# Performance work log

Measured on AMD Instinct MI355X. Metric: run time of the kernel, lower is better.

## Reference

```python
import jax, jax.numpy as jnp
import numpy as np

HID, OUT, HEADS, DIM_HEAD, TOPK, CHUNK = 512, 5, 8, 64, 8, 32
INNER = HEADS * DIM_HEAD  # 512
EPS = 1e-5


def setup_inputs():
    key = jax.random.key(0)
    ks = jax.random.split(key, 12)
    def p(k, shape, fan_in):
        return (jax.random.normal(k, shape, jnp.float32) / np.sqrt(fan_in).astype(np.float32))
    return {
        'x': jax.random.normal(ks[0], (32, 3, 32, 32), jnp.float32),
        'queries': jax.random.normal(ks[1], (4, 128, HID), jnp.float32),
        'memories': jax.random.normal(ks[2], (4, 20000, HID), jnp.float32),
        'mask': jnp.ones((4, 20000), bool),
        'conv1_w': p(ks[3], (16, 3, 3, 3), 27), 'conv1_b': jnp.zeros((16,), jnp.float32),
        'conv2_w': p(ks[4], (32, 16, 3, 3), 144), 'conv2_b': jnp.zeros((32,), jnp.float32),
        'fc1_w': p(ks[5], (32 * 8 * 8, HID), 2048), 'fc1_b': jnp.zeros((HID,), jnp.float32),
        'sq_w': p(ks[6], (HID, HID), HID), 'sq_b': jnp.zeros((HID,), jnp.float32),
        'sk_w': p(ks[7], (HID, HID), HID), 'sk_b': jnp.zeros((HID,), jnp.float32),
        'q_w': p(ks[8], (HID, INNER), HID),
        'kv_w': p(ks[9], (HID, 2 * INNER), HID),
        'out_w': p(ks[10], (INNER, HID), INNER), 'out_b': jnp.zeros((HID,), jnp.float32),
        'fc2_w': p(ks[11], (HID, OUT), HID), 'fc2_b': jnp.zeros((OUT,), jnp.float32),
    }


def _maxpool2(h):
    return jax.lax.reduce_window(h, -jnp.inf, jax.lax.max, (1, 1, 2, 2), (1, 1, 2, 2), 'VALID')


def _forward(x, queries, memories, mask, conv1_w, conv1_b, conv2_w, conv2_b,
             fc1_w, fc1_b, sq_w, sq_b, sk_w, sk_b, q_w, kv_w, out_w, out_b, fc2_w, fc2_b):
    # --- CNN branch: faithfully computed, but its output is discarded by the
    # original forward (x is overwritten by the attention output) ---
    dn = ('NCHW', 'OIHW', 'NCHW')
    h = jax.lax.conv_general_dilated(x, conv1_w, (1, 1), 'SAME', dimension_numbers=dn)
    h = _maxpool2(jax.nn.relu(h + conv1_b[None, :, None, None]))
    h = jax.lax.conv_general_dilated(h, conv2_w, (1, 1), 'SAME', dimension_numbers=dn)
    h = _maxpool2(jax.nn.relu(h + conv2_b[None, :, None, None]))
    h = h.reshape(h.shape[0], -1) @ fc1_w + fc1_b  # (B, 512), dead value (matches torch code)
    _ = h

    # --- HTMAttention ---
    b, qn, dim = queries.shape
    scale = dim ** -0.5  # chunk-scoring scale uses full dim
    mem = memories.reshape(b, -1, CHUNK, dim)            # (b, n, c, d)
    mk = mask.reshape(b, -1, CHUNK)                      # (b, n, c)

    # masked mean-pool summaries per chunk
    denom = mk.sum(-1, keepdims=True).astype(mem.dtype)  # (b, n, 1)
    summarized = jnp.where(mk[..., None], mem, 0.0).sum(2) / (denom + EPS)  # (b, n, d)

    sq = queries @ sq_w + sq_b                           # (b, i, d)
    sk = jax.lax.stop_gradient(summarized) @ sk_w + sk_b # (b, n, d)
    logits = jnp.einsum('bid,bnd->bin', sq, sk) * scale  # (b, i, n)
    neg = -jnp.finfo(logits.dtype).max
    logits = jnp.where(mk.any(-1)[:, None, :], logits, neg)

    topk_logits, topk_idx = jax.lax.top_k(logits, TOPK)  # (b, i, k)
    weights = jax.nn.softmax(topk_logits, axis=-1)       # (b, i, k)

    bidx = jnp.arange(b)[:, None, None]
    selected = mem[bidx, topk_idx]                       # (b, i, k, c, d) gather of chunks
    sel_mask = mk[bidx, topk_idx]                        # (b, i, k, c)

    # sinusoidal position over chunk positions (reversed arange, step-2 freqs)
    inv_freqs = 1e4 ** (-jnp.arange(0, dim, 2.0) / dim)              # (d/2,)
    sinu = jnp.arange(CHUNK - 1, -1, -1.0)[:, None] * inv_freqs      # (c, d/2)
    pos = jnp.concatenate([jnp.sin(sinu), jnp.cos(sinu)], -1)        # (c, d)
    selected = selected + pos

    # within-chunk multi-head attention (memories detached, as in original)
    mems_in = jax.lax.stop_gradient(selected)
    q = (queries @ q_w).reshape(b, qn, HEADS, DIM_HEAD) * (DIM_HEAD ** -0.5)  # (b,i,h,e)
    kv = (mems_in @ kv_w).reshape(b, qn, TOPK, CHUNK, 2, HEADS, DIM_HEAD)
    kk, vv = kv[..., 0, :, :], kv[..., 1, :, :]          # (b,i,k,c,h,e)

    sim = jnp.einsum('bihe,bikche->bhikc', q, kk)        # (b,h,i,k,c)
    sim = jnp.where(sel_mask[:, None], sim, neg)
    attn = jax.nn.softmax(sim, axis=-1)
    o = jnp.einsum('bhikc,bikche->bikhe', attn, vv).reshape(b, qn, TOPK, INNER)
    o = o @ out_w + out_b                                # (b, i, k, d)

    htm = (o * weights[..., None]).sum(2)                # (b, i, d)
    return htm @ fc2_w + fc2_b                           # (b, i, OUT)


def reference(x, queries, memories, mask, conv1_w, conv1_b, conv2_w, conv2_b,
              fc1_w, fc1_b, sq_w, sq_b, sk_w, sk_b, q_w, kv_w, out_w, out_b, fc2_w, fc2_b):
    return _forward(x, queries, memories, mask, conv1_w, conv1_b, conv2_w, conv2_b,
                    fc1_w, fc1_b, sq_w, sq_b, sk_w, sk_b, q_w, kv_w, out_w, out_b, fc2_w, fc2_b)
```

## Files before the change

kernel.cpp:

```cpp
#include <hip/hip_runtime.h>
#include <hip/hip_bf16.h>
#include <float.h>
#include <math.h>

#define NB      4
#define QN      128
#define HID     512
#define NMEM    20000
#define MPAD    20096
#define NCHUNK  625
#define CHUNK   32
#define HEADS   8
#define DHEAD   64
#define TOPKK   8
#define NKV     1024
#define GLD     64
#define LOGIT_SCALE 0.044194173824159216f
#define W2LD    576
#define STROWS  520
#define LGLD    640
#define TLD     4096

typedef __attribute__((ext_vector_type(8))) short bf16x8;
typedef __attribute__((ext_vector_type(4))) short bf16x4;
typedef __attribute__((ext_vector_type(4))) float f32x4;

__device__ __forceinline__ short f2bf(float f){
  __hip_bfloat16 h = __float2bfloat16(f);
  return *reinterpret_cast<short*>(&h);
}
__device__ __forceinline__ float bf2f(unsigned short s){
  __hip_bfloat16 h;
  *reinterpret_cast<unsigned short*>(&h) = s;
  return __bfloat162float(h);
}
__device__ __forceinline__ bool mask_at(const void* m, int flag, long i){
  return flag ? (((const unsigned char*)m)[i] != 0)
              : (((const int*)m)[i] != 0);
}
__device__ __forceinline__ void gload16(const void* g, void* l){
  __builtin_amdgcn_global_load_lds((const __attribute__((address_space(1))) void*)g,
                                   (__attribute__((address_space(3))) void*)l, 16, 0, 0);
}

__global__ __launch_bounds__(256) void bigsetup_kernel(const float* __restrict__ skw,
                                                       const void* __restrict__ mask,
                                                       const float* __restrict__ out_w,
                                                       const float* __restrict__ out_b,
                                                       const float* __restrict__ fc2_w,
                                                       const float* __restrict__ fc2_b,
                                                       const float* __restrict__ sq_w,
                                                       const float* __restrict__ sq_b,
                                                       const float* __restrict__ sk_b,
                                                       const float* __restrict__ q_w,
                                                       const float* __restrict__ kvw,
                                                       const float* __restrict__ queries,
                                                       float* __restrict__ skwT,
                                                       float* __restrict__ pos,
                                                       int* __restrict__ flagp,
                                                       float* __restrict__ bfold,
                                                       float* __restrict__ W2buf,
                                                       float* __restrict__ v2,
                                                       float* __restrict__ gbuf,
                                                       unsigned short* __restrict__ wqk,
                                                       unsigned short* __restrict__ qb,
                                                       unsigned short* __restrict__ PB){
  __shared__ float sm[12480];
  int sub = blockIdx.x;
  int t = threadIdx.x;
  if (sub < 64){
    float (*tile)[65] = (float(*)[65])sm;
    int c = t & 63, rbase = t >> 6;
    int e0 = (sub >> 3) * 64, j0 = (sub & 7) * 64;
#pragma unroll
    for (int j = 0; j < 16; ++j){
      int r = rbase + j * 4;
      tile[r][c] = skw[(long)(e0 + r) * 512 + j0 + c];
    }
    __syncthreads();
#pragma unroll
    for (int j = 0; j < 16; ++j){
      int rj = rbase + j * 4;
      skwT[(long)(j0 + rj) * 512 + e0 + c] = tile[c][rj];
    }
  } else if (sub < 128){
    int s = sub - 64;
    int cc = s >> 1;
    int d = (s & 1) * 256 + t;
    int j = (d < 256) ? d : d - 256;
    float invf = expf(-((2.0f * (float)j) / 512.0f) * 9.2103403719761836f);
    float arg = (float)(31 - cc) * invf;
    pos[cc * 512 + d] = (d < 256) ? sinf(arg) : cosf(arg);
    if (s == 0 && t == 0){
      const unsigned char* mb = (const unsigned char*)mask;
      *flagp = (mb[1] != 0) ? 1 : 0;
    }
  } else if (sub == 128){
    if (t < 5){
      float sb = 0.f;
      for (int k = 0; k < 512; ++k) sb += out_b[k] * fc2_w[k * 5 + t];
      bfold[t] = sb + fc2_b[t];
    }
  } else if (sub < 134){
    int s = sub - 129;
    if (s < 2){
      int d = s * 256 + t;
      float acc = 0.f;
      for (int j = 0; j < 512; ++j) acc += sq_w[(long)d * 512 + j] * sk_b[j];
      W2buf[(long)d * W2LD + 512] = acc;
      for (int cc = 513; cc < W2LD; ++cc) W2buf[(long)d * W2LD + cc] = 0.f;
    } else if (s < 4){
      int e = (s - 2) * 256 + t;
      float acc = 0.f;
      for (int j = 0; j < 512; ++j) acc += skw[(long)e * 512 + j] * sq_b[j];
      v2[e] = acc;
    } else {
      __shared__ float g[256];
      g[t] = sq_b[t] * sk_b[t] + sq_b[t + 256] * sk_b[t + 256];
      __syncthreads();
      for (int d = 128; d >= 1; d >>= 1){
        if (t < d) g[t] += g[t + d];
        __syncthreads();
      }
      if (t == 0) gbuf[0] = g[0];
    }
  } else if (sub < 390){
    int bx = sub - 134;
    int h = bx >> 5, rem2 = bx & 31, dp = rem2 >> 2, dd = rem2 & 3;
    int dpr0 = dp * 64, dd0 = dd * 128;
    float (*Akv)[65] = (float(*)[65])sm;
    float (*Bq)[65]  = (float(*)[65])(sm + 64 * 65);
    for (int idx = t; idx < 64 * 64; idx += 256){
      int r = idx >> 6, e = idx & 63;
      Akv[r][e] = kvw[(long)(dpr0 + r) * NKV + h * 64 + e];
    }
    for (int idx = t; idx < 128 * 64; idx += 256){
      int r = idx >> 6, e = idx & 63;
      Bq[r][e] = q_w[(long)(dd0 + r) * 512 + h * 64 + e];
    }
    __syncthreads();
    int ty = t >> 4, tx = t & 15;
    float acc[4][8] = {};
    for (int e = 0; e < 64; ++e){
      float a0 = Akv[ty * 4 + 0][e], a1 = Akv[ty * 4 + 1][e];
      float a2 = Akv[ty * 4 + 2][e], a3 = Akv[ty * 4 + 3][e];
      float b[8];
#pragma unroll
      for (int v = 0; v < 8; ++v) b[v] = Bq[tx * 8 + v][e];
#pragma unroll
      for (int v = 0; v < 8; ++v){
        acc[0][v] += a0 * b[v];
        acc[1][v] += a1 * b[v];
        acc[2][v] += a2 * b[v];
        acc[3][v] += a3 * b[v];
      }
    }
#pragma unroll
    for (int u = 0; u < 4; ++u)
#pragma unroll
      for (int v = 0; v < 8; ++v)
        wqk[(long)(h * 512 + dpr0 + ty * 4 + u) * 512 + dd0 + tx * 8 + v] =
            (unsigned short)f2bf(acc[u][v] * 0.125f);
  } else if (sub < 646){
    long idx = (long)(sub - 390) * 256 + t;
    float4 v = *(const float4*)(queries + idx * 4);
    ushort4 o;
    o.x = (unsigned short)f2bf(v.x);
    o.y = (unsigned short)f2bf(v.y);
    o.z = (unsigned short)f2bf(v.z);
    o.w = (unsigned short)f2bf(v.w);
    *(ushort4*)(qb + idx * 4) = o;
  } else {
    int row = sub - 646;
    if (row < 40){
      int h = row / 5, j = row - h * 5;
      __shared__ float wfc[64];
      if (t < 64){
        const float* owr = out_w + (long)(h * 64 + t) * 512;
        float s = 0.f;
        for (int k = 0; k < 512; ++k) s += owr[k] * fc2_w[k * 5 + j];
        wfc[t] = s;
      }
      __syncthreads();
      for (int d = t; d < 512; d += 256){
        const float* kr = kvw + (long)d * NKV + 512 + h * 64;
        float s = 0.f;
#pragma unroll
        for (int e = 0; e < 64; ++e) s += kr[e] * wfc[e];
        PB[(long)row * 512 + d] = (unsigned short)f2bf(s);
      }
    } else {
      for (int d = t; d < 512; d += 256) PB[(long)row * 512 + d] = 0;
    }
  }
}

__global__ __launch_bounds__(512) void prepsum_kernel(const float* __restrict__ memories,
                                                      const float* __restrict__ pos,
                                                      const void* __restrict__ mask,
                                                      const int* __restrict__ flagp,
                                                      unsigned short* __restrict__ abf_all,
                                                      float* __restrict__ summ,
                                                      float* __restrict__ chunkden){
  int n = blockIdx.x, b = blockIdx.y;
  int t = threadIdx.x;
  unsigned short* abf = abf_all + (long)b * MPAD * 512;
  if (n == NCHUNK){
    for (int idx = t; idx < 96 * 128; idx += 512){
      ushort4 z = {0, 0, 0, 0};
      *(ushort4*)(abf + (long)(NMEM + (idx >> 7)) * 512 + (long)(idx & 127) * 4) = z;
    }
    return;
  }
  long mbase = (long)b * NMEM + (long)n * CHUNK;
  int flag = *flagp;
  bool mybit = mask_at(mask, flag, mbase + (t & 31));
  unsigned int m32 = (unsigned int)__ballot(mybit);
  float den = (float)__popc(m32);
  int rh = t >> 6;
  int c8 = t & 63;
  const float* base = memories + mbase * HID + c8 * 8;
  const float* pbase = pos + c8 * 8;
  float4 va[4], vb[4], pa[4], pb[4];
#pragma unroll
  for (int j = 0; j < 4; ++j){
    va[j] = *(const float4*)(base + (long)(rh + 8 * j) * HID);
    vb[j] = *(const float4*)(base + (long)(rh + 8 * j) * HID + 4);
  }
#pragma unroll
  for (int j = 0; j < 4; ++j){
    pa[j] = *(const float4*)(pbase + (rh + 8 * j) * HID);
    pb[j] = *(const float4*)(pbase + (rh + 8 * j) * HID + 4);
  }
#pragma unroll
  for (int j = 0; j < 4; ++j){
    union { unsigned short u[8]; int4 v; } o;
    o.u[0] = (unsigned short)f2bf(va[j].x + pa[j].x);
    o.u[1] = (unsigned short)f2bf(va[j].y + pa[j].y);
    o.u[2] = (unsigned short)f2bf(va[j].z + pa[j].z);
    o.u[3] = (unsigned short)f2bf(va[j].w + pa[j].w);
    o.u[4] = (unsigned short)f2bf(vb[j].x + pb[j].x);
    o.u[5] = (unsigned short)f2bf(vb[j].y + pb[j].y);
    o.u[6] = (unsigned short)f2bf(vb[j].z + pb[j].z);
    o.u[7] = (unsigned short)f2bf(vb[j].w + pb[j].w);
    *(int4*)(abf + (long)(n * CHUNK + rh + 8 * j) * 512 + c8 * 8) = o.v;
  }
  float acc[8] = {};
#pragma unroll
  for (int j = 0; j < 4; ++j){
    if (m32 & (1u << (rh + 8 * j))){
      acc[0] += va[j].x; acc[1] += va[j].y; acc[2] += va[j].z; acc[3] += va[j].w;
      acc[4] += vb[j].x; acc[5] += vb[j].y; acc[6] += vb[j].z; acc[7] += vb[j].w;
    }
  }
  __shared__ float red[512][9];
#pragma unroll
  for (int k = 0; k < 8; ++k) red[t][k] = acc[k];
  __syncthreads();
  if (rh == 0){
    float s[8] = {};
    for (int g = 0; g < 8; ++g)
#pragma unroll
      for (int k = 0; k < 8; ++k) s[k] += red[g * 64 + c8][k];
    float dv = den + 1e-5f;
    float4 s0 = {s[0] / dv, s[1] / dv, s[2] / dv, s[3] / dv};
    float4 s1 = {s[4] / dv, s[5] / dv, s[6] / dv, s[7] / dv};
    float* srow = summ + ((long)b * NCHUNK + n) * 512 + c8 * 8;
    *(float4*)srow = s0;
    *(float4*)(srow + 4) = s1;
    if (t == 0) chunkden[b * NCHUNK + n] = den;
  }
}

__global__ __launch_bounds__(256) void gt_gemm(const unsigned short* __restrict__ abf_all,
                                               const unsigned short* __restrict__ PB,
                                               unsigned short* __restrict__ g_all,
                                               const unsigned short* __restrict__ Aq,
                                               const unsigned short* __restrict__ Bw,
                                               float* __restrict__ T,
                                               const float* __restrict__ sq_w,
                                               const float* __restrict__ skwT,
                                               float* __restrict__ W2buf){
  __shared__ unsigned short pool[20480];
  int blk = blockIdx.x;
  int tid = threadIdx.x, wid = tid >> 6, lane = tid & 63;
  int lr = lane & 15, lg = lane >> 4;
  int scol = (lane & 3) << 3;
  int srow = wid * 16 + (lane >> 2);

  if (blk < 316){
    int bb = blk / 79, g = blk - bb * 79;
    const unsigned short* A = abf_all + (size_t)bb * MPAD * 512;
    unsigned short* gout = g_all + (size_t)bb * MPAD * GLD;
    unsigned short* As[2] = { pool, pool + 8192 };
    unsigned short* Bs[2] = { pool + 16384, pool + 18432 };
    long rbase = (long)g * 256 + srow;
    long ra0 = rbase;       if (ra0 > MPAD - 1) ra0 = MPAD - 1;
    long ra1 = rbase + 64;  if (ra1 > MPAD - 1) ra1 = MPAD - 1;
    long ra2 = rbase + 128; if (ra2 > MPAD - 1) ra2 = MPAD - 1;
    long ra3 = rbase + 192; if (ra3 > MPAD - 1) ra3 = MPAD - 1;
    const unsigned short* gA0 = A + ra0 * 512 + scol;
    const unsigned short* gA1 = A + ra1 * 512 + scol;
    const unsigned short* gA2 = A + ra2 * 512 + scol;
    const unsigned short* gA3 = A + ra3 * 512 + scol;
    const unsigned short* gB0 = PB + (long)srow * 512 + scol;
    int lA0 = (wid * 16) * 32, lA1 = (64 + wid * 16) * 32;
    int lA2 = (128 + wid * 16) * 32, lA3 = (192 + wid * 16) * 32;
    int lB0 = (wid * 16) * 32;

    f32x4 acc[4][4];
#pragma unroll
    for (int i = 0; i < 4; ++i)
#pragma unroll
      for (int j = 0; j < 4; ++j) acc[i][j] = (f32x4)0.f;

#define GSTAGE(B, K0) { gload16(gA0 + (K0), &As[B][lA0]); gload16(gA1 + (K0), &As[B][lA1]); \
                        gload16(gA2 + (K0), &As[B][lA2]); gload16(gA3 + (K0), &As[B][lA3]); \
                        gload16(gB0 + (K0), &Bs[B][lB0]); }
#define GCOMPUTE(B) { bf16x8 af[4], bfv[4]; \
  _Pragma("unroll") for (int mi = 0; mi < 4; ++mi) af[mi]  = *(const bf16x8*)&As[B][(wid * 64 + mi * 16 + lr) * 32 + lg * 8]; \
  _Pragma("unroll") for (int ni = 0; ni < 4; ++ni) bfv[ni] = *(const bf16x8*)&Bs[B][(ni * 16 + lr) * 32 + lg * 8]; \
  _Pragma("unroll") for (int mi = 0; mi < 4; ++mi) \
    _Pragma("unroll") for (int ni = 0; ni < 4; ++ni) \
      acc[mi][ni] = __builtin_amdgcn_mfma_f32_16x16x32_bf16(af[mi], bfv[ni], acc[mi][ni], 0, 0, 0); }

    GSTAGE(0, 0);
    __syncthreads();
#pragma unroll 1
    for (int tt = 0; tt < 16; tt += 2){
      if (tt + 1 < 16) GSTAGE(1, (tt + 1) * 32);
      GCOMPUTE(0);
      __syncthreads();
      if (tt + 2 < 16) GSTAGE(0, (tt + 2) * 32);
      GCOMPUTE(1);
      __syncthreads();
    }
#undef GSTAGE
#undef GCOMPUTE

#pragma unroll
    for (int mi = 0; mi < 4; ++mi)
#pragma unroll
      for (int ni = 0; ni < 4; ++ni)
#pragma unroll
        for (int rr = 0; rr < 4; ++rr){
          long gr = (long)g * 256 + wid * 64 + mi * 16 + lg * 4 + rr;
          int gn = ni * 16 + lr;
          if (gr < MPAD)
            gout[gr * GLD + gn] = (unsigned short)f2bf(acc[mi][ni][rr]);
        }
  } else if (blk < 444){
    int L2 = blk - 316;
    int panel = L2 >> 5, nb = L2 & 31;
    int m0 = panel << 7, n0 = nb << 7;
    int wr = wid >> 1, wc = wid & 1;
    unsigned short* As[2] = { pool, pool + 4096 };
    unsigned short* Bs[2] = { pool + 8192, pool + 12288 };
    const unsigned short* gA0 = Aq + (long)(m0 + srow) * 512 + scol;
    const unsigned short* gA1 = gA0 + 64 * 512;
    const unsigned short* gB0 = Bw + (long)(n0 + srow) * 512 + scol;
    const unsigned short* gB1 = gB0 + 64 * 512;
    int lofs0 = (wid * 16) * 32;
    int lofs1 = (64 + wid * 16) * 32;

    f32x4 acc[4][4];
#pragma unroll
    for (int i = 0; i < 4; ++i)
#pragma unroll
      for (int j = 0; j < 4; ++j) acc[i][j] = (f32x4)0.f;

#define TSTAGE(B, K0) { gload16(gA0 + (K0), &As[B][lofs0]); gload16(gA1 + (K0), &As[B][lofs1]); \
                        gload16(gB0 + (K0), &Bs[B][lofs0]); gload16(gB1 + (K0), &Bs[B][lofs1]); }
#define TCOMPUTE(B) { bf16x8 af[4], bfv[4]; \
  _Pragma("unroll") for (int mi = 0; mi < 4; ++mi) af[mi]  = *(const bf16x8*)&As[B][(wr * 64 + mi * 16 + lr) * 32 + lg * 8]; \
  _Pragma("unroll") for (int ni = 0; ni < 4; ++ni) bfv[ni] = *(const bf16x8*)&Bs[B][(wc * 64 + ni * 16 + lr) * 32 + lg * 8]; \
  _Pragma("unroll") for (int mi = 0; mi < 4; ++mi) \
    _Pragma("unroll") for (int ni = 0; ni < 4; ++ni) \
      acc[mi][ni] = __builtin_amdgcn_mfma_f32_16x16x32_bf16(af[mi], bfv[ni], acc[mi][ni], 0, 0, 0); }

    TSTAGE(0, 0);
    __syncthreads();
#pragma unroll 1
    for (int tt = 0; tt < 16; tt += 2){
      if (tt + 1 < 16) TSTAGE(1, (tt + 1) * 32);
      TCOMPUTE(0);
      __syncthreads();
      if (tt + 2 < 16) TSTAGE(0, (tt + 2) * 32);
      TCOMPUTE(1);
      __syncthreads();
    }
#undef TSTAGE
#undef TCOMPUTE

#pragma unroll
    for (int mi = 0; mi < 4; ++mi)
#pragma unroll
      for (int ni = 0; ni < 4; ++ni)
#pragma unroll
        for (int rr = 0; rr < 4; ++rr){
          int gr = m0 + wr * 64 + mi * 16 + lg * 4 + rr;
          int gn = n0 + wc * 64 + ni * 16 + lr;
          T[(long)gr * TLD + gn] = acc[mi][ni][rr];
        }
  } else {
    int bx3 = blk - 444;
    int rt = bx3 & 63, nt2 = bx3 >> 6;
    int r0 = rt * 8 + wid * 2;
    int nn = nt2 * 64 + lane;
    const float* a0 = sq_w + (long)r0 * 512;
    const float* bp = skwT + nn;
    float acc0 = 0.f, acc1 = 0.f;
#pragma unroll 4
    for (int k = 0; k < 512; k += 4){
      float b0 = bp[(long)k * 512];
      float b1 = bp[(long)(k + 1) * 512];
      float b2 = bp[(long)(k + 2) * 512];
      float b3 = bp[(long)(k + 3) * 512];
      float4 a;
      a = *(const float4*)(a0 + k);
      acc0 += a.x * b0 + a.y * b1 + a.z * b2 + a.w * b3;
      a = *(const float4*)(a0 + 512 + k);
      acc1 += a.x * b0 + a.y * b1 + a.z * b2 + a.w * b3;
    }
    W2buf[(long)r0 * W2LD + nn]       = acc0;
    W2buf[(long)(r0 + 1) * W2LD + nn] = acc1;
  }
}

__global__ __launch_bounds__(256) void ustb_kernel(const float* __restrict__ queries,
                                                   const float* __restrict__ W2buf,
                                                   float* __restrict__ u_ext,
                                                   const float* __restrict__ summ,
                                                   const float* __restrict__ v2,
                                                   const float* __restrict__ gbuf,
                                                   float* __restrict__ summText,
                                                   float* __restrict__ betag){
  int blk = blockIdx.x;
  int t = threadIdx.x;
  if (blk < 576){
    int ax = blk & 63, ay = blk >> 6;
    int lane = t & 63, w = t >> 6;
    int r0 = ax * 8 + w * 2;
    int n  = ay * 64 + lane;
    const float* a0 = queries + (long)r0 * 512;
    const float* bp = W2buf + n;
    float acc0 = 0.f, acc1 = 0.f;
#pragma unroll 4
    for (int k = 0; k < 512; k += 4){
      float b0 = bp[(long)k * W2LD];
      float b1 = bp[(long)(k + 1) * W2LD];
      float b2 = bp[(long)(k + 2) * W2LD];
      float b3 = bp[(long)(k + 3) * W2LD];
      float4 a;
      a = *(const float4*)(a0 + k);
      acc0 += a.x * b0 + a.y * b1 + a.z * b2 + a.w * b3;
      a = *(const float4*)(a0 + 512 + k);
      acc1 += a.x * b0 + a.y * b1 + a.z * b2 + a.w * b3;
    }
    u_ext[(long)r0 * W2LD + n]       = acc0;
    u_ext[(long)(r0 + 1) * W2LD + n] = acc1;
  } else if (blk < 896){
    __shared__ float tile[64][65];
    int b2 = blk - 576;
    int b = b2 / 80; int rem = b2 % 80;
    int n0 = (rem / 8) * 64, e0 = (rem % 8) * 64;
    int c = t & 63, rbase = t >> 6;
#pragma unroll
    for (int j = 0; j < 16; ++j){
      int r = rbase + j * 4;
      int n = n0 + r;
      tile[r][c] = (n < NCHUNK) ? summ[((long)b * NCHUNK + n) * 512 + e0 + c] : 0.f;
    }
    __syncthreads();
#pragma unroll
    for (int j = 0; j < 16; ++j){
      int re = rbase + j * 4;
      summText[(long)b * STROWS * LGLD + (long)(e0 + re) * LGLD + n0 + c] = tile[c][re];
    }
  } else if (blk < 900){
    int b = blk - 896;
    for (int idx = t; idx < 8 * LGLD; idx += 256){
      int e = idx / LGLD, n = idx - e * LGLD;
      summText[(long)b * STROWS * LGLD + (long)(512 + e) * LGLD + n] = (e == 0) ? 1.f : 0.f;
    }
  } else {
    int bb = blk - 900;
    int w = t >> 6, lane = t & 63;
    int row = bb * 4 + w;
    const float* r = summ + (long)row * 512;
    float s = 0.f;
#pragma unroll
    for (int c = 0; c < 8; ++c) s += r[lane + 64 * c] * v2[lane + 64 * c];
    for (int d = 32; d >= 1; d >>= 1) s += __shfl_xor(s, d, 64);
    if (lane == 0){
      int b = row / NCHUNK, n = row % NCHUNK;
      betag[b * LGLD + n] = s + gbuf[0];
    }
  }
}

__global__ __launch_bounds__(256) void logits_nn(const float* __restrict__ u_ext,
                                                 const float* __restrict__ summText,
                                                 const float* __restrict__ betag,
                                                 const float* __restrict__ chunkden,
                                                 float* __restrict__ logits){
  int b = blockIdx.z;
  int tid = threadIdx.x;
  int lane = tid & 63, w = tid >> 6;
  int r0 = blockIdx.x * 8 + w * 2;
  int n  = blockIdx.y * 64 + lane;
  const float* a0 = u_ext + ((long)b * QN + r0) * W2LD;
  const float* bp = summText + (long)b * STROWS * LGLD + n;
  float acc0 = 0.f, acc1 = 0.f;
#pragma unroll 4
  for (int k = 0; k < STROWS; k += 4){
    float b0 = bp[(long)k * LGLD];
    float b1 = bp[(long)(k + 1) * LGLD];
    float b2 = bp[(long)(k + 2) * LGLD];
    float b3 = bp[(long)(k + 3) * LGLD];
    float4 a;
    a = *(const float4*)(a0 + k);
    acc0 += a.x * b0 + a.y * b1 + a.z * b2 + a.w * b3;
    a = *(const float4*)(a0 + W2LD + k);
    acc1 += a.x * b0 + a.y * b1 + a.z * b2 + a.w * b3;
  }
  if (n < NCHUNK){
    float bet = betag[b * LGLD + n];
    bool dead = (chunkden[b * NCHUNK + n] <= 0.f);
    float v0 = (acc0 + bet) * LOGIT_SCALE;
    float v1 = (acc1 + bet) * LOGIT_SCALE;
    if (dead){ v0 = v1 = -FLT_MAX; }
    long base = ((long)b * QN + r0) * LGLD + n;
    logits[base]        = v0;
    logits[base + LGLD] = v1;
  }
}

__global__ __launch_bounds__(256) void topk_kernel(const float* __restrict__ logits,
                                                   int* __restrict__ topi_out,
                                                   float* __restrict__ wts_out){
  int row = blockIdx.x;
  __shared__ float lds[NCHUNK];
  __shared__ float wv[4];
  __shared__ int   wi[4];
  __shared__ float topv[TOPKK];
  __shared__ int   topi[TOPKK];
  int t = threadIdx.x;
  int lane = t & 63, w = t >> 6;
  for (int idx = t; idx < NCHUNK; idx += 256) lds[idx] = logits[(long)row * LGLD + idx];
  __syncthreads();
  for (int it = 0; it < TOPKK; ++it){
    float bv = -INFINITY; int bi = 0x7fffffff;
    for (int idx = t; idx < NCHUNK; idx += 256){
      float v = lds[idx];
      if (v > bv){ bv = v; bi = idx; }
    }
    for (int d = 32; d >= 1; d >>= 1){
      float ov = __shfl_xor(bv, d, 64);
      int   oi = __shfl_xor(bi, d, 64);
      if (ov > bv || (ov == bv && oi < bi)){ bv = ov; bi = oi; }
    }
    if (lane == 0){ wv[w] = bv; wi[w] = bi; }
    __syncthreads();
    if (t == 0){
      float fb = wv[0]; int fi = wi[0];
      for (int j = 1; j < 4; ++j){
        if (wv[j] > fb || (wv[j] == fb && wi[j] < fi)){ fb = wv[j]; fi = wi[j]; }
      }
      topv[it] = fb; topi[it] = fi; lds[fi] = -INFINITY;
    }
    __syncthreads();
  }
  if (t == 0){
    float m = topv[0];
    for (int r = 1; r < TOPKK; ++r) m = fmaxf(m, topv[r]);
    float e[TOPKK], s = 0.f;
    for (int r = 0; r < TOPKK; ++r){ e[r] = expf(topv[r] - m); s += e[r]; }
    for (int r = 0; r < TOPKK; ++r){
      wts_out[(long)row * TOPKK + r] = e[r] / s;
      topi_out[(long)row * TOPKK + r] = topi[r];
    }
  }
}

#define ALDP 516
__global__ __launch_bounds__(256) void attn5_kernel(const float* __restrict__ T,
                                                    const unsigned short* __restrict__ abf_all,
                                                    const unsigned short* __restrict__ g_all,
                                                    const int* __restrict__ topidx,
                                                    const float* __restrict__ wts,
                                                    const void* __restrict__ mask,
                                                    const int* __restrict__ flagp,
                                                    float* __restrict__ osc5){
  int bx = blockIdx.x;
  int bb = bx >> 10, rem = bx & 1023;
  int i = rem >> 3, k = rem & 7;
  const unsigned short* abf = abf_all + (size_t)bb * MPAD * 512;
  const unsigned short* gb  = g_all + (size_t)bb * MPAD * GLD;
  int t = threadIdx.x;
  __shared__ unsigned short A_lds[32 * ALDP];
  __shared__ float T_lds[TLD];
  __shared__ float red[4][5];
  int flag = *flagp;
  long sel = ((long)(bb * QN + i)) * TOPKK + k;
  int chunk = topidx[sel];
  float w8 = wts[sel];
  const float* Trow = T + (long)(bb * QN + i) * TLD;
  for (int idx = t; idx < 1024; idx += 256)
    *(float4*)&T_lds[idx * 4] = *(const float4*)&Trow[idx * 4];
  {
    int r = t >> 3, cb = (t & 7) * 64;
    const unsigned short* src = abf + (long)(chunk * CHUNK + r) * 512 + cb;
    unsigned short* dst = &A_lds[r * ALDP + cb];
#pragma unroll
    for (int j = 0; j < 8; ++j){
      bf16x8 a8 = *(const bf16x8*)(src + j * 8);
      bf16x4 lo = {a8[0], a8[1], a8[2], a8[3]};
      bf16x4 hi = {a8[4], a8[5], a8[6], a8[7]};
      *(bf16x4*)(dst + j * 8)     = lo;
      *(bf16x4*)(dst + j * 8 + 4) = hi;
    }
  }
  __syncthreads();
  int h = t >> 5, c = t & 31;
  const unsigned short* arow = &A_lds[c * ALDP];
  const float* tp = &T_lds[h * 512];
  float s = 0.f;
#pragma unroll 4
  for (int e8 = 0; e8 < 64; ++e8){
    bf16x4 alo = *(const bf16x4*)(arow + e8 * 8);
    bf16x4 ahi = *(const bf16x4*)(arow + e8 * 8 + 4);
    float4 ta = *(const float4*)(tp + e8 * 8);
    float4 tb = *(const float4*)(tp + e8 * 8 + 4);
    s += bf2f((unsigned short)alo[0]) * ta.x + bf2f((unsigned short)alo[1]) * ta.y
       + bf2f((unsigned short)alo[2]) * ta.z + bf2f((unsigned short)alo[3]) * ta.w
       + bf2f((unsigned short)ahi[0]) * tb.x + bf2f((unsigned short)ahi[1]) * tb.y
       + bf2f((unsigned short)ahi[2]) * tb.z + bf2f((unsigned short)ahi[3]) * tb.w;
  }
  bool mv = mask_at(mask, flag, (long)bb * NMEM + (long)chunk * CHUNK + c);
  if (!mv) s = -FLT_MAX;
  float m = s;
  for (int d = 16; d >= 1; d >>= 1) m = fmaxf(m, __shfl_xor(m, d, 32));
  float p = expf(s - m);
  float su = p;
  for (int d = 16; d >= 1; d >>= 1) su += __shfl_xor(su, d, 32);
  float att = p / su;
  const unsigned short* grow = gb + (long)(chunk * CHUNK + c) * GLD + h * 5;
  float p0 = att * bf2f(grow[0]);
  float p1 = att * bf2f(grow[1]);
  float p2 = att * bf2f(grow[2]);
  float p3 = att * bf2f(grow[3]);
  float p4 = att * bf2f(grow[4]);
#pragma unroll
  for (int d = 32; d >= 1; d >>= 1){
    p0 += __shfl_xor(p0, d, 64);
    p1 += __shfl_xor(p1, d, 64);
    p2 += __shfl_xor(p2, d, 64);
    p3 += __shfl_xor(p3, d, 64);
    p4 += __shfl_xor(p4, d, 64);
  }
  int w = t >> 6, lane = t & 63;
  if (lane == 0){
    red[w][0] = p0; red[w][1] = p1; red[w][2] = p2; red[w][3] = p3; red[w][4] = p4;
  }
  __syncthreads();
  if (t < 5){
    float tot = red[0][t] + red[1][t] + red[2][t] + red[3][t];
    osc5[sel * 8 + t] = w8 * tot;
  }
}

__global__ __launch_bounds__(64) void final5_kernel(const float* __restrict__ osc5,
                                                    const float* __restrict__ bfold,
                                                    float* __restrict__ out){
  int bi = blockIdx.x;
  int t = threadIdx.x;
  if (t < 5){
    float a = bfold[t];
#pragma unroll
    for (int k = 0; k < TOPKK; ++k) a += osc5[((long)bi * TOPKK + k) * 8 + t];
    out[bi * 5 + t] = a;
  }
}

extern "C" void kernel_launch(void* const* d_in, const int* in_sizes, int n_in,
                              void* d_out, int out_size, void* d_ws, size_t ws_size,
                              hipStream_t stream) {
  const float* queries  = (const float*)d_in[1];
  const float* memories = (const float*)d_in[2];
  const void*  mask     = d_in[3];
  const float* sq_w = (const float*)d_in[10];
  const float* sq_b = (const float*)d_in[11];
  const float* sk_w = (const float*)d_in[12];
  const float* sk_b = (const float*)d_in[13];
  const float* q_w  = (const float*)d_in[14];
  const float* kv_w = (const float*)d_in[15];
  const float* out_w = (const float*)d_in[16];
  const float* out_b = (const float*)d_in[17];
  const float* fc2_w = (const float*)d_in[18];
  const float* fc2_b = (const float*)d_in[19];
  float* out = (float*)d_out;

  char* ws = (char*)d_ws;
  size_t off = 0;
  auto alloc = [&](size_t bytes){ size_t o = off; off += (bytes + 511) & ~(size_t)511; return o; };
  size_t o_sum  = alloc(5120000);
  size_t o_den  = alloc(10240);
  size_t o_pos  = alloc(65536);
  size_t o_bf   = alloc(512);
  size_t o_ti   = alloc(16384);
  size_t o_wt   = alloc(16384);
  size_t o_flag = alloc(512);
  size_t o_w2   = alloc(1179648);
  size_t o_uex  = alloc(1179648);
  size_t o_st   = alloc(5324800);
  size_t o_bg   = alloc(10240);
  size_t o_v2   = alloc(2048);
  size_t o_gm   = alloc(512);
  size_t o_lg   = alloc(1310720);
  size_t o_osc5 = alloc(131072);
  size_t o_skt  = alloc(1048576);
  size_t o_qbf  = alloc(524288);
  size_t o_wqk  = alloc(4194304);
  size_t o_T    = alloc((size_t)NB * QN * TLD * 4);
  size_t o_pb   = alloc(65536);
  size_t o_abf  = alloc((size_t)NB * MPAD * 512 * 2);
  size_t o_g    = alloc((size_t)NB * MPAD * GLD * 2);

  float* summ  = (float*)(ws + o_sum);
  float* den   = (float*)(ws + o_den);
  float* pos   = (float*)(ws + o_pos);
  float* bfold = (float*)(ws + o_bf);
  int*   ti    = (int*)  (ws + o_ti);
  float* wt    = (float*)(ws + o_wt);
  int*   flagp = (int*)  (ws + o_flag);
  float* W2buf = (float*)(ws + o_w2);
  float* u_ext = (float*)(ws + o_uex);
  float* summText = (float*)(ws + o_st);
  float* betag = (float*)(ws + o_bg);
  float* v2    = (float*)(ws + o_v2);
  float* gbuf  = (float*)(ws + o_gm);
  float* logit = (float*)(ws + o_lg);
  float* osc5  = (float*)(ws + o_osc5);
  float* skwT  = (float*)(ws + o_skt);
  unsigned short* qb   = (unsigned short*)(ws + o_qbf);
  unsigned short* wqk  = (unsigned short*)(ws + o_wqk);
  float* Tbuf  = (float*)(ws + o_T);
  unsigned short* PB   = (unsigned short*)(ws + o_pb);
  unsigned short* abf  = (unsigned short*)(ws + o_abf);
  unsigned short* gall = (unsigned short*)(ws + o_g);

  bigsetup_kernel<<<dim3(710), dim3(256), 0, stream>>>(
      sk_w, mask, out_w, out_b, fc2_w, fc2_b, sq_w, sq_b, sk_b, q_w, kv_w, queries,
      skwT, pos, flagp, bfold, W2buf, v2, gbuf, wqk, qb, PB);

  prepsum_kernel<<<dim3(NCHUNK + 1, NB), dim3(512), 0, stream>>>(
      memories, pos, mask, flagp, abf, summ, den);

  gt_gemm<<<dim3(956), dim3(256), 0, stream>>>(
      abf, PB, gall, qb, wqk, Tbuf, sq_w, skwT, W2buf);

  ustb_kernel<<<dim3(1525), dim3(256), 0, stream>>>(
      queries, W2buf, u_ext, summ, v2, gbuf, summText, betag);
  logits_nn<<<dim3(16, 10, NB), dim3(256), 0, stream>>>(u_ext, summText, betag, den, logit);
  topk_kernel<<<dim3(NB * QN), dim3(256), 0, stream>>>(logit, ti, wt);

  attn5_kernel<<<dim3(NB * QN * TOPKK), dim3(256), 0, stream>>>(
      Tbuf, abf, gall, ti, wt, mask, flagp, osc5);
  final5_kernel<<<dim3(NB * QN), dim3(64), 0, stream>>>(osc5, bfold, out);
}
```

Measured before the change: 275.5 us.

## Fold summary transpose into GEMM launch and fuse attention with final reduction

The summary-transpose, constant-row fill and beta dot-product blocks move out of the old ustb kernel and into the gt_gemm launch, because they do not depend on W2buf. The remaining u_ext GEMM becomes its own small kernel. The per-(query, topk) attention kernel and the final reduction kernel are merged: one block per query loops over the 8 selected chunks, loads the T row into LDS once, and writes the output directly. This removes a launch, the osc5 round trip and the repeated T loads. The cost is 8x fewer attention blocks, each doing serial work, which lowers parallelism.

```diff
diff --git a/kernel.cpp b/kernel.cpp
--- a/kernel.cpp
+++ b/kernel.cpp
@@ -280,7 +280,12 @@
                                                float* __restrict__ T,
                                                const float* __restrict__ sq_w,
                                                const float* __restrict__ skwT,
-                                               float* __restrict__ W2buf){
+                                               float* __restrict__ W2buf,
+                                               const float* __restrict__ summ,
+                                               const float* __restrict__ v2,
+                                               const float* __restrict__ gbuf,
+                                               float* __restrict__ summText,
+                                               float* __restrict__ betag){
   __shared__ unsigned short pool[20480];
   int blk = blockIdx.x;
   int tid = threadIdx.x, wid = tid >> 6, lane = tid & 63;
@@ -402,7 +407,7 @@
           int gn = n0 + wc * 64 + ni * 16 + lr;
           T[(long)gr * TLD + gn] = acc[mi][ni][rr];
         }
-  } else {
+  } else if (blk < 956){
     int bx3 = blk - 444;
     int rt = bx3 & 63, nt2 = bx3 >> 6;
     int r0 = rt * 8 + wid * 2;
@@ -424,79 +429,74 @@
     }
     W2buf[(long)r0 * W2LD + nn]       = acc0;
     W2buf[(long)(r0 + 1) * W2LD + nn] = acc1;
-  }
-}
-
-__global__ __launch_bounds__(256) void ustb_kernel(const float* __restrict__ queries,
+  } else {
+    int sb = blk - 956;
+    int t = tid;
+    if (sb < 320){
+      float (*tile)[65] = (float(*)[65])pool;
+      int b = sb / 80; int rem = sb % 80;
+      int n0 = (rem / 8) * 64, e0 = (rem % 8) * 64;
+      int c = t & 63, rbase = t >> 6;
+#pragma unroll
+      for (int j = 0; j < 16; ++j){
+        int r = rbase + j * 4;
+        int n = n0 + r;
+        tile[r][c] = (n < NCHUNK) ? summ[((long)b * NCHUNK + n) * 512 + e0 + c] : 0.f;
+      }
+      __syncthreads();
+#pragma unroll
+      for (int j = 0; j < 16; ++j){
+        int re = rbase + j * 4;
+        summText[(long)b * STROWS * LGLD + (long)(e0 + re) * LGLD + n0 + c] = tile[c][re];
+      }
+    } else if (sb < 324){
+      int b = sb - 320;
+      for (int idx = t; idx < 8 * LGLD; idx += 256){
+        int e = idx / LGLD, n = idx - e * LGLD;
+        summText[(long)b * STROWS * LGLD + (long)(512 + e) * LGLD + n] = (e == 0) ? 1.f : 0.f;
+      }
+    } else {
+      int bb2 = sb - 324;
+      int row = bb2 * 4 + wid;
+      const float* r = summ + (long)row * 512;
+      float s = 0.f;
+#pragma unroll
+      for (int c = 0; c < 8; ++c) s += r[lane + 64 * c] * v2[lane + 64 * c];
+      for (int d = 32; d >= 1; d >>= 1) s += __shfl_xor(s, d, 64);
+      if (lane == 0){
+        int b = row / NCHUNK, n = row % NCHUNK;
+        betag[b * LGLD + n] = s + gbuf[0];
+      }
+    }
+  }
+}
+
+__global__ __launch_bounds__(256) void uext_kernel(const float* __restrict__ queries,
                                                    const float* __restrict__ W2buf,
-                                                   float* __restrict__ u_ext,
-                                                   const float* __restrict__ summ,
-                                                   const float* __restrict__ v2,
-                                                   const float* __restrict__ gbuf,
-                                                   float* __restrict__ summText,
-                                                   float* __restrict__ betag){
+                                                   float* __restrict__ u_ext){
   int blk = blockIdx.x;
   int t = threadIdx.x;
-  if (blk < 576){
-    int ax = blk & 63, ay = blk >> 6;
-    int lane = t & 63, w = t >> 6;
-    int r0 = ax * 8 + w * 2;
-    int n  = ay * 64 + lane;
-    const float* a0 = queries + (long)r0 * 512;
-    const float* bp = W2buf + n;
-    float acc0 = 0.f, acc1 = 0.f;
+  int ax = blk & 63, ay = blk >> 6;
+  int lane = t & 63, w = t >> 6;
+  int r0 = ax * 8 + w * 2;
+  int n  = ay * 64 + lane;
+  const float* a0 = queries + (long)r0 * 512;
+  const float* bp = W2buf + n;
+  float acc0 = 0.f, acc1 = 0.f;
 #pragma unroll 4
-    for (int k = 0; k < 512; k += 4){
-      float b0 = bp[(long)k * W2LD];
-      float b1 = bp[(long)(k + 1) * W2LD];
-      float b2 = bp[(long)(k + 2) * W2LD];
-      float b3 = bp[(long)(k + 3) * W2LD];
-      float4 a;
-      a = *(const float4*)(a0 + k);
-      acc0 += a.x * b0 + a.y * b1 + a.z * b2 + a.w * b3;
-      a = *(const float4*)(a0 + 512 + k);
-      acc1 += a.x * b0 + a.y * b1 + a.z * b2 + a.w * b3;
-    }
-    u_ext[(long)r0 * W2LD + n]       = acc0;
-    u_ext[(long)(r0 + 1) * W2LD + n] = acc1;
-  } else if (blk < 896){
-    __shared__ float tile[64][65];
-    int b2 = blk - 576;
-    int b = b2 / 80; int rem = b2 % 80;
-    int n0 = (rem / 8) * 64, e0 = (rem % 8) * 64;
-    int c = t & 63, rbase = t >> 6;
-#pragma unroll
-    for (int j = 0; j < 16; ++j){
-      int r = rbase + j * 4;
-      int n = n0 + r;
-      tile[r][c] = (n < NCHUNK) ? summ[((long)b * NCHUNK + n) * 512 + e0 + c] : 0.f;
-    }
-    __syncthreads();
-#pragma unroll
-    for (int j = 0; j < 16; ++j){
-      int re = rbase + j * 4;
-      summText[(long)b * STROWS * LGLD + (long)(e0 + re) * LGLD + n0 + c] = tile[c][re];
-    }
-  } else if (blk < 900){
-    int b = blk - 896;
-    for (int idx = t; idx < 8 * LGLD; idx += 256){
-      int e = idx / LGLD, n = idx - e * LGLD;
-      summText[(long)b * STROWS * LGLD + (long)(512 + e) * LGLD + n] = (e == 0) ? 1.f : 0.f;
-    }
-  } else {
-    int bb = blk - 900;
-    int w = t >> 6, lane = t & 63;
-    int row = bb * 4 + w;
-    const float* r = summ + (long)row * 512;
-    float s = 0.f;
-#pragma unroll
-    for (int c = 0; c < 8; ++c) s += r[lane + 64 * c] * v2[lane + 64 * c];
-    for (int d = 32; d >= 1; d >>= 1) s += __shfl_xor(s, d, 64);
-    if (lane == 0){
-      int b = row / NCHUNK, n = row % NCHUNK;
-      betag[b * LGLD + n] = s + gbuf[0];
-    }
-  }
+  for (int k = 0; k < 512; k += 4){
+    float b0 = bp[(long)k * W2LD];
+    float b1 = bp[(long)(k + 1) * W2LD];
+    float b2 = bp[(long)(k + 2) * W2LD];
+    float b3 = bp[(long)(k + 3) * W2LD];
+    float4 a;
+    a = *(const float4*)(a0 + k);
+    acc0 += a.x * b0 + a.y * b1 + a.z * b2 + a.w * b3;
+    a = *(const float4*)(a0 + 512 + k);
+    acc1 += a.x * b0 + a.y * b1 + a.z * b2 + a.w * b3;
+  }
+  u_ext[(long)r0 * W2LD + n]       = acc0;
+  u_ext[(long)(r0 + 1) * W2LD + n] = acc1;
 }
 
 __global__ __launch_bounds__(256) void logits_nn(const float* __restrict__ u_ext,
@@ -584,17 +584,17 @@
 }
 
 #define ALDP 516
-__global__ __launch_bounds__(256) void attn5_kernel(const float* __restrict__ T,
-                                                    const unsigned short* __restrict__ abf_all,
-                                                    const unsigned short* __restrict__ g_all,
-                                                    const int* __restrict__ topidx,
-                                                    const float* __restrict__ wts,
-                                                    const void* __restrict__ mask,
-                                                    const int* __restrict__ flagp,
-                                                    float* __restrict__ osc5){
+__global__ __launch_bounds__(256) void attn_fused(const float* __restrict__ T,
+                                                  const unsigned short* __restrict__ abf_all,
+                                                  const unsigned short* __restrict__ g_all,
+                                                  const int* __restrict__ topidx,
+                                                  const float* __restrict__ wts,
+                                                  const void* __restrict__ mask,
+                                                  const int* __restrict__ flagp,
+                                                  const float* __restrict__ bfold,
+                                                  float* __restrict__ out){
   int bx = blockIdx.x;
-  int bb = bx >> 10, rem = bx & 1023;
-  int i = rem >> 3, k = rem & 7;
+  int bb = bx >> 7, i = bx & 127;
   const unsigned short* abf = abf_all + (size_t)bb * MPAD * 512;
   const unsigned short* gb  = g_all + (size_t)bb * MPAD * GLD;
   int t = threadIdx.x;
@@ -602,85 +602,78 @@
   __shared__ float T_lds[TLD];
   __shared__ float red[4][5];
   int flag = *flagp;
-  long sel = ((long)(bb * QN + i)) * TOPKK + k;
-  int chunk = topidx[sel];
-  float w8 = wts[sel];
+  long selbase = ((long)(bb * QN + i)) * TOPKK;
   const float* Trow = T + (long)(bb * QN + i) * TLD;
   for (int idx = t; idx < 1024; idx += 256)
     *(float4*)&T_lds[idx * 4] = *(const float4*)&Trow[idx * 4];
-  {
-    int r = t >> 3, cb = (t & 7) * 64;
-    const unsigned short* src = abf + (long)(chunk * CHUNK + r) * 512 + cb;
-    unsigned short* dst = &A_lds[r * ALDP + cb];
-#pragma unroll
-    for (int j = 0; j < 8; ++j){
-      bf16x8 a8 = *(const bf16x8*)(src + j * 8);
-      bf16x4 lo = {a8[0], a8[1], a8[2], a8[3]};
-      bf16x4 hi = {a8[4], a8[5], a8[6], a8[7]};
-      *(bf16x4*)(dst + j * 8)     = lo;
-      *(bf16x4*)(dst + j * 8 + 4) = hi;
-    }
-  }
-  __syncthreads();
+  float acc5 = (t < 5) ? bfold[t] : 0.f;
   int h = t >> 5, c = t & 31;
-  const unsigned short* arow = &A_lds[c * ALDP];
-  const float* tp = &T_lds[h * 512];
-  float s = 0.f;
+  int w = t >> 6, lane = t & 63;
+  int sr = t >> 3, scb = (t & 7) * 64;
+
+#pragma unroll 1
+  for (int k = 0; k < TOPKK; ++k){
+    int chunk = topidx[selbase + k];
+    float w8 = wts[selbase + k];
+    {
+      const unsigned short* src = abf + (long)(chunk * CHUNK + sr) * 512 + scb;
+      unsigned short* dst = &A_lds[sr * ALDP + scb];
+#pragma unroll
+      for (int j = 0; j < 8; ++j){
+        bf16x8 a8 = *(const bf16x8*)(src + j * 8);
+        bf16x4 lo = {a8[0], a8[1], a8[2], a8[3]};
+        bf16x4 hi = {a8[4], a8[5], a8[6], a8[7]};
+        *(bf16x4*)(dst + j * 8)     = lo;
+        *(bf16x4*)(dst + j * 8 + 4) = hi;
+      }
+    }
+    __syncthreads();
+    const unsigned short* arow = &A_lds[c * ALDP];
+    const float* tp = &T_lds[h * 512];
+    float s = 0.f;
 #pragma unroll 4
-  for (int e8 = 0; e8 < 64; ++e8){
-    bf16x4 alo = *(const bf16x4*)(arow + e8 * 8);
-    bf16x4 ahi = *(const bf16x4*)(arow + e8 * 8 + 4);
-    float4 ta = *(const float4*)(tp + e8 * 8);
-    float4 tb = *(const float4*)(tp + e8 * 8 + 4);
-    s += bf2f((unsigned short)alo[0]) * ta.x + bf2f((unsigned short)alo[1]) * ta.y
-       + bf2f((unsigned short)alo[2]) * ta.z + bf2f((unsigned short)alo[3]) * ta.w
-       + bf2f((unsigned short)ahi[0]) * tb.x + bf2f((unsigned short)ahi[1]) * tb.y
-       + bf2f((unsigned short)ahi[2]) * tb.z + bf2f((unsigned short)ahi[3]) * tb.w;
-  }
-  bool mv = mask_at(mask, flag, (long)bb * NMEM + (long)chunk * CHUNK + c);
-  if (!mv) s = -FLT_MAX;
-  float m = s;
-  for (int d = 16; d >= 1; d >>= 1) m = fmaxf(m, __shfl_xor(m, d, 32));
-  float p = expf(s - m);
-  float su = p;
-  for (int d = 16; d >= 1; d >>= 1) su += __shfl_xor(su, d, 32);
-  float att = p / su;
-  const unsigned short* grow = gb + (long)(chunk * CHUNK + c) * GLD + h * 5;
-  float p0 = att * bf2f(grow[0]);
-  float p1 = att * bf2f(grow[1]);
-  float p2 = att * bf2f(grow[2]);
-  float p3 = att * bf2f(grow[3]);
-  float p4 = att * bf2f(grow[4]);
-#pragma unroll
-  for (int d = 32; d >= 1; d >>= 1){
-    p0 += __shfl_xor(p0, d, 64);
-    p1 += __shfl_xor(p1, d, 64);
-    p2 += __shfl_xor(p2, d, 64);
-    p3 += __shfl_xor(p3, d, 64);
-    p4 += __shfl_xor(p4, d, 64);
-  }
-  int w = t >> 6, lane = t & 63;
-  if (lane == 0){
-    red[w][0] = p0; red[w][1] = p1; red[w][2] = p2; red[w][3] = p3; red[w][4] = p4;
-  }
-  __syncthreads();
-  if (t < 5){
-    float tot = red[0][t] + red[1][t] + red[2][t] + red[3][t];
-    osc5[sel * 8 + t] = w8 * tot;
-  }
-}
-
-__global__ __launch_bounds__(64) void final5_kernel(const float* __restrict__ osc5,
-                                                    const float* __restrict__ bfold,
-                                                    float* __restrict__ out){
-  int bi = blockIdx.x;
-  int t = threadIdx.x;
-  if (t < 5){
-    float a = bfold[t];
-#pragma unroll
-    for (int k = 0; k < TOPKK; ++k) a += osc5[((long)bi * TOPKK + k) * 8 + t];
-    out[bi * 5 + t] = a;
-  }
+    for (int e8 = 0; e8 < 64; ++e8){
+      bf16x4 alo = *(const bf16x4*)(arow + e8 * 8);
+      bf16x4 ahi = *(const bf16x4*)(arow + e8 * 8 + 4);
+      float4 ta = *(const float4*)(tp + e8 * 8);
+      float4 tb = *(const float4*)(tp + e8 * 8 + 4);
+      s += bf2f((unsigned short)alo[0]) * ta.x + bf2f((unsigned short)alo[1]) * ta.y
+         + bf2f((unsigned short)alo[2]) * ta.z + bf2f((unsigned short)alo[3]) * ta.w
+         + bf2f((unsigned short)ahi[0]) * tb.x + bf2f((unsigned short)ahi[1]) * tb.y
+         + bf2f((unsigned short)ahi[2]) * tb.z + bf2f((unsigned short)ahi[3]) * tb.w;
+    }
+    bool mv = mask_at(mask, flag, (long)bb * NMEM + (long)chunk * CHUNK + c);
+    if (!mv) s = -FLT_MAX;
+    float m = s;
+    for (int d = 16; d >= 1; d >>= 1) m = fmaxf(m, __shfl_xor(m, d, 32));
+    float p = expf(s - m);
+    float su = p;
+    for (int d = 16; d >= 1; d >>= 1) su += __shfl_xor(su, d, 32);
+    float att = p / su;
+    const unsigned short* grow = gb + (long)(chunk * CHUNK + c) * GLD + h * 5;
+    float p0 = att * bf2f(grow[0]);
+    float p1 = att * bf2f(grow[1]);
+    float p2 = att * bf2f(grow[2]);
+    float p3 = att * bf2f(grow[3]);
+    float p4 = att * bf2f(grow[4]);
+#pragma unroll
+    for (int d = 32; d >= 1; d >>= 1){
+      p0 += __shfl_xor(p0, d, 64);
+      p1 += __shfl_xor(p1, d, 64);
+      p2 += __shfl_xor(p2, d, 64);
+      p3 += __shfl_xor(p3, d, 64);
+      p4 += __shfl_xor(p4, d, 64);
+    }
+    if (lane == 0){
+      red[w][0] = p0; red[w][1] = p1; red[w][2] = p2; red[w][3] = p3; red[w][4] = p4;
+    }
+    __syncthreads();
+    if (t < 5){
+      float tot = red[0][t] + red[1][t] + red[2][t] + red[3][t];
+      acc5 += w8 * tot;
+    }
+  }
+  if (t < 5) out[(long)(bb * QN + i) * 5 + t] = acc5;
 }
 
 extern "C" void kernel_launch(void* const* d_in, const int* in_sizes, int n_in,
@@ -718,7 +711,6 @@
   size_t o_v2   = alloc(2048);
   size_t o_gm   = alloc(512);
   size_t o_lg   = alloc(1310720);
-  size_t o_osc5 = alloc(131072);
   size_t o_skt  = alloc(1048576);
   size_t o_qbf  = alloc(524288);
   size_t o_wqk  = alloc(4194304);
@@ -741,7 +733,6 @@
   float* v2    = (float*)(ws + o_v2);
   float* gbuf  = (float*)(ws + o_gm);
   float* logit = (float*)(ws + o_lg);
-  float* osc5  = (float*)(ws + o_osc5);
   float* skwT  = (float*)(ws + o_skt);
   unsigned short* qb   = (unsigned short*)(ws + o_qbf);
   unsigned short* wqk  = (unsigned short*)(ws + o_wqk);
@@ -757,15 +748,13 @@
   prepsum_kernel<<<dim3(NCHUNK + 1, NB), dim3(512), 0, stream>>>(
       memories, pos, mask, flagp, abf, summ, den);
 
-  gt_gemm<<<dim3(956), dim3(256), 0, stream>>>(
-      abf, PB, gall, qb, wqk, Tbuf, sq_w, skwT, W2buf);
-
-  ustb_kernel<<<dim3(1525), dim3(256), 0, stream>>>(
-      queries, W2buf, u_ext, summ, v2, gbuf, summText, betag);
+  gt_gemm<<<dim3(1905), dim3(256), 0, stream>>>(
+      abf, PB, gall, qb, wqk, Tbuf, sq_w, skwT, W2buf, summ, v2, gbuf, summText, betag);
+
+  uext_kernel<<<dim3(576), dim3(256), 0, stream>>>(queries, W2buf, u_ext);
   logits_nn<<<dim3(16, 10, NB), dim3(256), 0, stream>>>(u_ext, summText, betag, den, logit);
   topk_kernel<<<dim3(NB * QN), dim3(256), 0, stream>>>(logit, ti, wt);
 
-  attn5_kernel<<<dim3(NB * QN * TOPKK), dim3(256), 0, stream>>>(
-      Tbuf, abf, gall, ti, wt, mask, flagp, osc5);
-  final5_kernel<<<dim3(NB * QN), dim3(64), 0, stream>>>(osc5, bfold, out);
-}
+  attn_fused<<<dim3(NB * QN), dim3(256), 0, stream>>>(
+      Tbuf, abf, gall, ti, wt, mask, flagp, bfold, out);
+}
```

After: 284.9 us. +3.4%, slower.
